# Kernel tuning notes

Hardware: AMD Instinct MI355X
Metric: run time of the kernel (lower is better)

Reference implementation:

```python
import jax, jax.numpy as jnp
import numpy as np

NUM_HEADS = 16
ROPE_BASE = 10000.0


def _rope_tables(seq_len, head_dim, dtype=jnp.float32):
    # Standard RoPE: inv_freq over even dims, cos/sin of shape [seq, head_dim]
    inv_freq = 1.0 / (ROPE_BASE ** (jnp.arange(0, head_dim, 2, dtype=jnp.float32) / head_dim))
    freqs = jnp.arange(seq_len, dtype=jnp.float32)[:, None] * inv_freq[None, :]  # [S, hd/2]
    emb = jnp.concatenate([freqs, freqs], axis=-1)  # [S, hd]
    return jnp.cos(emb).astype(dtype), jnp.sin(emb).astype(dtype)


def _apply_rope(t, cos, sin):
    # t: [B, H, S, hd]; cos/sin: [S, hd]
    half = t.shape[-1] // 2
    rot = jnp.concatenate([-t[..., half:], t[..., :half]], axis=-1)
    return t * cos[None, None, :, :] + rot * sin[None, None, :, :]


def setup_inputs() -> dict:
    key = jax.random.key(0)
    ks = jax.random.split(key, 7)
    B, S, D, L = 2, 2048, 2048, 256
    sc = lambda fan_in: 1.0 / np.sqrt(fan_in)
    return {
        "x": jax.random.normal(ks[0], (B, S, D), jnp.float32),
        "wq": jax.random.normal(ks[1], (D, D), jnp.float32) * sc(D),
        "wdkv": jax.random.normal(ks[2], (L, D), jnp.float32) * sc(D),
        "wuk": jax.random.normal(ks[3], (D, L), jnp.float32) * sc(L),
        "wuv": jax.random.normal(ks[4], (D, L), jnp.float32) * sc(L),
        "wo": jax.random.normal(ks[5], (D, D), jnp.float32) * sc(D),
        "bo": jnp.zeros((D,), jnp.float32),
    }


def reference(x, wq, wdkv, wuk, wuv, wo, bo):
    B, S, D = x.shape
    H = NUM_HEADS
    hd = wq.shape[0] // H

    # Projections (torch nn.Linear: y = x @ W.T)
    q = jnp.einsum("bsd,ed->bse", x, wq)          # [B, S, D]
    latent = jnp.einsum("bsd,ld->bsl", x, wdkv)   # [B, S, L]
    k = jnp.einsum("bsl,el->bse", latent, wuk)    # [B, S, D]
    v = jnp.einsum("bsl,el->bse", latent, wuv)    # [B, S, D]

    split = lambda t: t.reshape(B, S, H, hd).transpose(0, 2, 1, 3)  # [B, H, S, hd]
    q, k, v = split(q), split(k), split(v)

    cos, sin = _rope_tables(S, hd, x.dtype)
    q = _apply_rope(q, cos, sin)
    k = _apply_rope(k, cos, sin)

    scores = jnp.einsum("bhqd,bhkd->bhqk", q, k) / jnp.sqrt(jnp.asarray(hd, x.dtype))
    causal = jnp.tril(jnp.ones((S, S), bool))
    scores = jnp.where(causal[None, None], scores, jnp.asarray(-jnp.inf, x.dtype))
    attn = jax.nn.softmax(scores, axis=-1)

    ctx = jnp.einsum("bhqk,bhkd->bhqd", attn, v)
    ctx = ctx.transpose(0, 2, 1, 3).reshape(B, S, H * hd)
    return jnp.einsum("bse,oe->bso", ctx, wo) + bo
```

## Files before the change

### kernel.cpp

```cpp
#include <hip/hip_runtime.h>
#include <hip/hip_bf16.h>

typedef __bf16 bf16;
typedef __bf16 bf16x8 __attribute__((ext_vector_type(8)));
typedef __bf16 bf16x4 __attribute__((ext_vector_type(4)));
typedef float  f32x4  __attribute__((ext_vector_type(4)));
typedef float  f32x16 __attribute__((ext_vector_type(16)));
typedef unsigned int u32x4 __attribute__((ext_vector_type(4)));

#define D_MODEL 2048
#define SEQ     2048
#define BATCH   2
#define NHEAD   16
#define HDIM    128
#define LATENT  256
#define BROWS   SEQ

typedef __attribute__((address_space(1))) void gvoid;
typedef __attribute__((address_space(3))) void svoid;

__device__ __forceinline__ void gld16(const bf16* g, bf16* l) {
  __builtin_amdgcn_global_load_lds((gvoid*)(void*)g, (svoid*)l, 16, 0, 0);
}

__device__ __forceinline__ f32x4 mfma16(bf16x8 a, bf16x8 b, f32x4 c) {
  return __builtin_amdgcn_mfma_f32_16x16x32_bf16(a, b, c, 0, 0, 0);
}
__device__ __forceinline__ f32x16 mfma32(bf16x8 a, bf16x8 b, f32x16 c) {
  return __builtin_amdgcn_mfma_f32_32x32x16_bf16(a, b, c, 0, 0, 0);
}

__device__ __forceinline__ unsigned cvt_pk_bf16(float lo, float hi) {
  unsigned r;
  asm("v_cvt_pk_bf16_f32 %0, %1, %2" : "=v"(r) : "v"(lo), "v"(hi));
  return r;
}

__device__ __forceinline__ float fw(float v) {
  union { float f; unsigned u; } x; x.f = v;
  if ((x.u & 0x7f800000u) == 0x7f800000u) return 0.f;
  return v;
}

template<typename T>
__device__ __forceinline__ bf16x8 ld_cvt8(const T* p);
template<>
__device__ __forceinline__ bf16x8 ld_cvt8<float>(const float* p) {
  const float4 a = *(const float4*)p;
  const float4 b = *(const float4*)(p + 4);
  bf16x8 r;
  r[0] = (bf16)a.x; r[1] = (bf16)a.y; r[2] = (bf16)a.z; r[3] = (bf16)a.w;
  r[4] = (bf16)b.x; r[5] = (bf16)b.y; r[6] = (bf16)b.z; r[7] = (bf16)b.w;
  return r;
}
template<>
__device__ __forceinline__ bf16x8 ld_cvt8<bf16>(const bf16* p) {
  return *(const bf16x8*)p;
}

template<typename TC>
__device__ __forceinline__ void st_c(TC* p, float v);
template<> __device__ __forceinline__ void st_c<bf16>(bf16* p, float v)   { *p = (bf16)v; }
template<> __device__ __forceinline__ void st_c<float>(float* p, float v) { *p = v; }

__global__ __launch_bounds__(256)
void cvt_bf16(const float* __restrict__ in, bf16* __restrict__ out, int n8)
{
  int i = blockIdx.x * 256 + threadIdx.x;
  if (i >= n8) return;
  const float4 a = ((const float4*)in)[2 * i];
  const float4 b = ((const float4*)in)[2 * i + 1];
  bf16x8 r;
  r[0] = (bf16)a.x; r[1] = (bf16)a.y; r[2] = (bf16)a.z; r[3] = (bf16)a.w;
  r[4] = (bf16)b.x; r[5] = (bf16)b.y; r[6] = (bf16)b.z; r[7] = (bf16)b.w;
  ((bf16x8*)out)[i] = r;
}

template<typename TA, typename TW, typename TC, int BIAS, int TRANSC>
__global__ __launch_bounds__(256)
void gemm_nt(const TA* __restrict__ A, const TW* __restrict__ W,
             TC* __restrict__ C, const float* __restrict__ bias,
             int M, int N, int K)
{
  const int t    = threadIdx.x;
  const int wave = t >> 6, lane = t & 63;
  const int quad = lane >> 4, l16 = lane & 15;
  const int wr = (wave >> 1) * 64, wc = (wave & 1) * 64;
  const int am0 = blockIdx.x * 128;
  const int bn0 = blockIdx.y * 128;

  __shared__ __align__(16) bf16 As[128][40];
  __shared__ __align__(16) bf16 Bs[128][40];

  const f32x4 fzero = {0.f, 0.f, 0.f, 0.f};
  f32x4 acc[4][4];
#pragma unroll
  for (int i = 0; i < 4; i++)
#pragma unroll
    for (int j = 0; j < 4; j++) acc[i][j] = fzero;

  const int srow = t >> 2;
  const int scol = (t & 3) * 8;

  for (int k0 = 0; k0 < K; k0 += 32) {
#pragma unroll
    for (int c = 0; c < 2; c++) {
      int row = srow + c * 64;
      *(bf16x8*)(&As[row][scol]) =
        ld_cvt8<TA>(A + (size_t)(am0 + row) * K + k0 + scol);
      *(bf16x8*)(&Bs[row][scol]) =
        ld_cvt8<TW>(W + (size_t)(bn0 + row) * K + k0 + scol);
    }
    __syncthreads();

    bf16x8 af[4], bfr[4];
#pragma unroll
    for (int i = 0; i < 4; i++)
      af[i]  = *(const bf16x8*)(&As[wr + i*16 + l16][quad*8]);
#pragma unroll
    for (int j = 0; j < 4; j++)
      bfr[j] = *(const bf16x8*)(&Bs[wc + j*16 + l16][quad*8]);
#pragma unroll
    for (int i = 0; i < 4; i++)
#pragma unroll
      for (int j = 0; j < 4; j++)
        acc[i][j] = mfma16(af[i], bfr[j], acc[i][j]);
    __syncthreads();
  }

#pragma unroll
  for (int i = 0; i < 4; i++) {
#pragma unroll
    for (int j = 0; j < 4; j++) {
      int col = bn0 + wc + j*16 + l16;
      float bv = 0.f;
      if (BIAS) bv = bias[col];
#pragma unroll
      for (int r = 0; r < 4; r++) {
        int row = am0 + wr + i*16 + quad*4 + r;
        if (TRANSC)
          st_c<TC>(&C[(size_t)col * M + row], fw(acc[i][j][r] + bv));
        else
          st_c<TC>(&C[(size_t)row * N + col], fw(acc[i][j][r] + bv));
      }
    }
  }
}

template<typename TC, int BIAS, int TRANSC>
__global__ __launch_bounds__(256)
void gemm_bb(const bf16* __restrict__ A, const bf16* __restrict__ W,
             TC* __restrict__ C, const float* __restrict__ bias,
             int M, int N, int K)
{
  const int t    = threadIdx.x;
  const int wave = t >> 6, lane = t & 63;
  const int quad = lane >> 4, l16 = lane & 15;
  const int wr = (wave >> 1) * 64, wc = (wave & 1) * 64;
  const int am0 = blockIdx.x * 128;
  const int bn0 = blockIdx.y * 128;

  __shared__ __align__(16) bf16 As[128 * 32];
  __shared__ __align__(16) bf16 Bs[128 * 32];

  const f32x4 fzero = {0.f, 0.f, 0.f, 0.f};
  f32x4 acc[4][4];
#pragma unroll
  for (int i = 0; i < 4; i++)
#pragma unroll
    for (int j = 0; j < 4; j++) acc[i][j] = fzero;

  for (int k0 = 0; k0 < K; k0 += 32) {
#pragma unroll
    for (int c = 0; c < 2; c++) {
      int e   = c * 256 + t;
      int row = e >> 2, col = (e & 3) * 8;
      gld16(A + (size_t)(am0 + row) * K + k0 + col, As + e * 8);
      gld16(W + (size_t)(bn0 + row) * K + k0 + col, Bs + e * 8);
    }
    __syncthreads();

    bf16x8 af[4], bfr[4];
#pragma unroll
    for (int i = 0; i < 4; i++)
      af[i]  = *(const bf16x8*)(As + (size_t)(wr + i*16 + l16) * 32 + quad * 8);
#pragma unroll
    for (int j = 0; j < 4; j++)
      bfr[j] = *(const bf16x8*)(Bs + (size_t)(wc + j*16 + l16) * 32 + quad * 8);
#pragma unroll
    for (int i = 0; i < 4; i++)
#pragma unroll
      for (int j = 0; j < 4; j++)
        acc[i][j] = mfma16(af[i], bfr[j], acc[i][j]);
    __syncthreads();
  }

#pragma unroll
  for (int i = 0; i < 4; i++) {
#pragma unroll
    for (int j = 0; j < 4; j++) {
      int col = bn0 + wc + j*16 + l16;
      float bv = 0.f;
      if (BIAS) bv = bias[col];
#pragma unroll
      for (int r = 0; r < 4; r++) {
        int row = am0 + wr + i*16 + quad*4 + r;
        if (TRANSC)
          st_c<TC>(&C[(size_t)col * M + row], fw(acc[i][j][r] + bv));
        else
          st_c<TC>(&C[(size_t)row * N + col], fw(acc[i][j][r] + bv));
      }
    }
  }
}

template<typename TC, int BIAS, int TRANSC>
__global__ __launch_bounds__(256)
void gemm_bf(const bf16* __restrict__ A, const float* __restrict__ W,
             TC* __restrict__ C, const float* __restrict__ bias,
             int M, int N, int K)
{
  const int t    = threadIdx.x;
  const int wave = t >> 6, lane = t & 63;
  const int quad = lane >> 4, l16 = lane & 15;
  const int wr = (wave >> 1) * 64, wc = (wave & 1) * 64;
  const int am0 = blockIdx.x * 128;
  const int bn0 = blockIdx.y * 128;

  __shared__ __align__(16) bf16 As[128 * 32];
  __shared__ __align__(16) bf16 Bs[128][40];

  const f32x4 fzero = {0.f, 0.f, 0.f, 0.f};
  f32x4 acc[4][4];
#pragma unroll
  for (int i = 0; i < 4; i++)
#pragma unroll
    for (int j = 0; j < 4; j++) acc[i][j] = fzero;

  const int srow = t >> 2;
  const int scol = (t & 3) * 8;

  for (int k0 = 0; k0 < K; k0 += 32) {
#pragma unroll
    for (int c = 0; c < 2; c++) {
      int e   = c * 256 + t;
      int row = e >> 2, col = (e & 3) * 8;
      gld16(A + (size_t)(am0 + row) * K + k0 + col, As + e * 8);
      int brow = srow + c * 64;
      *(bf16x8*)(&Bs[brow][scol]) =
        ld_cvt8<float>(W + (size_t)(bn0 + brow) * K + k0 + scol);
    }
    __syncthreads();

    bf16x8 af[4], bfr[4];
#pragma unroll
    for (int i = 0; i < 4; i++)
      af[i]  = *(const bf16x8*)(As + (size_t)(wr + i*16 + l16) * 32 + quad * 8);
#pragma unroll
    for (int j = 0; j < 4; j++)
      bfr[j] = *(const bf16x8*)(&Bs[wc + j*16 + l16][quad*8]);
#pragma unroll
    for (int i = 0; i < 4; i++)
#pragma unroll
      for (int j = 0; j < 4; j++)
        acc[i][j] = mfma16(af[i], bfr[j], acc[i][j]);
    __syncthreads();
  }

#pragma unroll
  for (int i = 0; i < 4; i++) {
#pragma unroll
    for (int j = 0; j < 4; j++) {
      int col = bn0 + wc + j*16 + l16;
      float bv = 0.f;
      if (BIAS) bv = bias[col];
#pragma unroll
      for (int r = 0; r < 4; r++) {
        int row = am0 + wr + i*16 + quad*4 + r;
        if (TRANSC)
          st_c<TC>(&C[(size_t)col * M + row], fw(acc[i][j][r] + bv));
        else
          st_c<TC>(&C[(size_t)row * N + col], fw(acc[i][j][r] + bv));
      }
    }
  }
}

template<int SPLITK>
__global__ __launch_bounds__(256)
void gemm_bf_sk(const bf16* __restrict__ A, const float* __restrict__ W,
                float* __restrict__ Cp, int M, int N, int K)
{
  const int t    = threadIdx.x;
  const int wave = t >> 6, lane = t & 63;
  const int quad = lane >> 4, l16 = lane & 15;
  const int wr = (wave >> 1) * 64, wc = (wave & 1) * 64;
  const int am0 = blockIdx.x * 128;
  const int bn0 = blockIdx.y * 128;
  const int kbeg = blockIdx.z * (K / SPLITK);
  const int kend = kbeg + K / SPLITK;

  __shared__ __align__(16) bf16 As[128 * 32];
  __shared__ __align__(16) bf16 Bs[128][40];

  const f32x4 fzero = {0.f, 0.f, 0.f, 0.f};
  f32x4 acc[4][4];
#pragma unroll
  for (int i = 0; i < 4; i++)
#pragma unroll
    for (int j = 0; j < 4; j++) acc[i][j] = fzero;

  const int srow = t >> 2;
  const int scol = (t & 3) * 8;

  for (int k0 = kbeg; k0 < kend; k0 += 32) {
#pragma unroll
    for (int c = 0; c < 2; c++) {
      int e   = c * 256 + t;
      int row = e >> 2, col = (e & 3) * 8;
      gld16(A + (size_t)(am0 + row) * K + k0 + col, As + e * 8);
      int brow = srow + c * 64;
      *(bf16x8*)(&Bs[brow][scol]) =
        ld_cvt8<float>(W + (size_t)(bn0 + brow) * K + k0 + scol);
    }
    __syncthreads();

    bf16x8 af[4], bfr[4];
#pragma unroll
    for (int i = 0; i < 4; i++)
      af[i]  = *(const bf16x8*)(As + (size_t)(wr + i*16 + l16) * 32 + quad * 8);
#pragma unroll
    for (int j = 0; j < 4; j++)
      bfr[j] = *(const bf16x8*)(&Bs[wc + j*16 + l16][quad*8]);
#pragma unroll
    for (int i = 0; i < 4; i++)
#pragma unroll
      for (int j = 0; j < 4; j++)
        acc[i][j] = mfma16(af[i], bfr[j], acc[i][j]);
    __syncthreads();
  }

  float* Cb = Cp + (size_t)blockIdx.z * M * N;
#pragma unroll
  for (int i = 0; i < 4; i++)
#pragma unroll
    for (int j = 0; j < 4; j++) {
      int col = bn0 + wc + j*16 + l16;
#pragma unroll
      for (int r = 0; r < 4; r++) {
        int row = am0 + wr + i*16 + quad*4 + r;
        Cb[(size_t)row * N + col] = acc[i][j][r];
      }
    }
}

template<int SPLITK>
__global__ __launch_bounds__(256)
void reduce_sk(const float* __restrict__ Cp, bf16* __restrict__ out, int MN)
{
  int i4 = (blockIdx.x * 256 + threadIdx.x) * 4;
  if (i4 >= MN) return;
  float4 s = *(const float4*)(Cp + i4);
#pragma unroll
  for (int k = 1; k < SPLITK; k++) {
    float4 p = *(const float4*)(Cp + (size_t)k * MN + i4);
    s.x += p.x; s.y += p.y; s.z += p.z; s.w += p.w;
  }
  bf16x4 o;
  o[0] = (bf16)fw(s.x); o[1] = (bf16)fw(s.y);
  o[2] = (bf16)fw(s.z); o[3] = (bf16)fw(s.w);
  *(bf16x4*)(out + i4) = o;
}

__global__ __launch_bounds__(256)
void rope_kernel(bf16* __restrict__ Q, bf16* __restrict__ Kr)
{
  int idx = blockIdx.x * 256 + threadIdx.x;
  int j   = idx & 63;
  int h   = (idx >> 6) & 15;
  int row = idx >> 10;
  int s   = row & (SEQ - 1);

  float invf = exp2f(-0.2076205059304601f * (float)j);
  float ang  = (float)s * invf;
  float c = cosf(ang), si = sinf(ang);

  size_t base = (size_t)row * D_MODEL + h * HDIM;
  float q1 = (float)Q[base + j], q2 = (float)Q[base + j + 64];
  Q[base + j]      = (bf16)(q1 * c - q2 * si);
  Q[base + j + 64] = (bf16)(q2 * c + q1 * si);
  float k1 = (float)Kr[base + j], k2 = (float)Kr[base + j + 64];
  Kr[base + j]      = (bf16)(k1 * c - k2 * si);
  Kr[base + j + 64] = (bf16)(k2 * c + k1 * si);
}

__global__ __launch_bounds__(256, 2)
void flash_attn(const bf16* __restrict__ Q, const bf16* __restrict__ Kc,
                const bf16* __restrict__ VT, bf16* __restrict__ O, int ldVT)
{
  const int L    = blockIdx.x;
  const int half = L >> 8;
  const int Mn   = L & 255;
  const int h    = Mn >> 4;
  const int a    = Mn & 15;
  const int qt   = half ? 15 - a : a;
  const int b    = half;
  const int t    = threadIdx.x;
  const int wave = t >> 6, lane = t & 63;
  const int m31  = lane & 31, hi = lane >> 5;
  const int rowbase = b * SEQ;

  __shared__ __align__(16) bf16 Ks[64 * 128];
  __shared__ __align__(16) bf16 Vs[128 * 64];

  bf16x8 qf[8];
  {
    const bf16* qp = Q + (size_t)(rowbase + qt*128 + wave*32 + m31) * D_MODEL
                   + h * HDIM + hi * 8;
#pragma unroll
    for (int dk = 0; dk < 8; dk++)
      qf[dk] = *(const bf16x8*)(qp + dk * 16);
  }

  f32x16 oacc[4];
#pragma unroll
  for (int db = 0; db < 4; db++)
#pragma unroll
    for (int i = 0; i < 16; i++) oacc[db][i] = 0.f;
  float lsum = 0.f;

  const float SC2 = 0.12752051581562927f;

  const int ktmax = 2*qt + 1;
  const bf16* kbase0 = Kc + (size_t)rowbase * D_MODEL + h * HDIM;
  const bf16* vbase0 = VT + (size_t)(h*HDIM) * ldVT + rowbase;

  bf16x8 kr[4], vr[4];
#pragma unroll
  for (int c = 0; c < 4; c++) {
    int e = c*256 + t;
    kr[c] = *(const bf16x8*)(kbase0 + (size_t)(e >> 4) * D_MODEL + (e & 15) * 8);
    vr[c] = *(const bf16x8*)(vbase0 + (size_t)(e >> 3) * ldVT + (e & 7) * 8);
  }

  for (int kt = 0; kt <= ktmax; kt++) {
#pragma unroll
    for (int c = 0; c < 4; c++) {
      int e = c*256 + t;
      int krow = e >> 4, kch = e & 15;
      *(bf16x8*)(Ks + krow * 128 + ((kch ^ (krow & 7)) * 8)) = kr[c];
      int vrow = e >> 3, vch = e & 7;
      *(bf16x8*)(Vs + vrow * 64  + ((vch ^ (vrow & 7)) * 8)) = vr[c];
    }
    __syncthreads();

    if (kt < ktmax) {
      const bf16* kb = kbase0 + (size_t)((kt+1)*64) * D_MODEL;
      const bf16* vb = vbase0 + (kt+1)*64;
#pragma unroll
      for (int c = 0; c < 4; c++) {
        int e = c*256 + t;
        kr[c] = *(const bf16x8*)(kb + (size_t)(e >> 4) * D_MODEL + (e & 15) * 8);
        vr[c] = *(const bf16x8*)(vb + (size_t)(e >> 3) * ldVT + (e & 7) * 8);
      }
    }

    const int kvoff = kt*64 - qt*128;
    const bool activ = (kvoff < 0) | (kvoff <= wave*32 + 31);

    if (activ) {
      unsigned pb[4][4];
#pragma unroll
      for (int kb = 0; kb < 2; kb++) {
        f32x16 s;
#pragma unroll
        for (int i = 0; i < 16; i++) s[i] = 0.f;
        const int krow = kb*32 + m31;
        const bf16* ksrow = Ks + krow * 128;
        const int swz = (krow & 7);
#pragma unroll
        for (int dk = 0; dk < 8; dk++) {
          bf16x8 kf = *(const bf16x8*)(ksrow + (((dk*2 + hi) ^ swz) * 8));
          s = mfma32(kf, qf[dk], s);
        }

        float p[16];
        const int kq = kvoff + kb*32 + 4*hi - (wave*32 + m31);
#pragma unroll
        for (int r = 0; r < 16; r++) {
          float v = s[r] * SC2;
          const int kk = (r & 3) + 8 * (r >> 2);
          if (kvoff >= 0 && (kq + kk) > 0) v = -1e30f;
          float e2 = exp2f(v);
          lsum += e2;
          p[r] = e2;
        }

#pragma unroll
        for (int c = 0; c < 2; c++) {
          unsigned a0 = cvt_pk_bf16(p[(2*c)*4 + 0],   p[(2*c)*4 + 1]);
          unsigned a1 = cvt_pk_bf16(p[(2*c)*4 + 2],   p[(2*c)*4 + 3]);
          unsigned b0 = cvt_pk_bf16(p[(2*c+1)*4 + 0], p[(2*c+1)*4 + 1]);
          unsigned b1 = cvt_pk_bf16(p[(2*c+1)*4 + 2], p[(2*c+1)*4 + 3]);
          asm("v_permlane32_swap_b32 %0, %1" : "+v"(a0), "+v"(b0));
          asm("v_permlane32_swap_b32 %0, %1" : "+v"(a1), "+v"(b1));
          pb[kb*2 + c][0] = a0; pb[kb*2 + c][1] = a1;
          pb[kb*2 + c][2] = b0; pb[kb*2 + c][3] = b1;
        }
      }

#pragma unroll
      for (int db = 0; db < 4; db++) {
        const int vrow = db*32 + m31;
        const bf16* vsrow = Vs + vrow * 64;
        const int swz = (vrow & 7);
#pragma unroll
        for (int kc = 0; kc < 4; kc++) {
          bf16x8 vf = *(const bf16x8*)(vsrow + (((kc*2 + hi) ^ swz) * 8));
          u32x4 w = {pb[kc][0], pb[kc][1], pb[kc][2], pb[kc][3]};
          oacc[db] = mfma32(vf, __builtin_bit_cast(bf16x8, w), oacc[db]);
        }
      }
    }
    __syncthreads();
  }

  const float ltot = lsum + __shfl_xor(lsum, 32, 64);
  const float invl = 1.f / ltot;
  const size_t ob = (size_t)(rowbase + qt*128 + wave*32 + m31) * D_MODEL + h * HDIM;
#pragma unroll
  for (int db = 0; db < 4; db++) {
#pragma unroll
    for (int q2 = 0; q2 < 4; q2++) {
      bf16x4 o4;
#pragma unroll
      for (int rr = 0; rr < 4; rr++)
        o4[rr] = (bf16)(oacc[db][q2*4 + rr] * invl);
      *(bf16x4*)(O + ob + db*32 + q2*8 + hi*4) = o4;
    }
  }
}

extern "C" void kernel_launch(void* const* d_in, const int* in_sizes, int n_in,
                              void* d_out, int out_size, void* d_ws, size_t ws_size,
                              hipStream_t stream)
{
  const float* x    = (const float*)d_in[0];
  const float* wq   = (const float*)d_in[1];
  const float* wdkv = (const float*)d_in[2];
  const float* wuk  = (const float*)d_in[3];
  const float* wuv  = (const float*)d_in[4];
  const float* wo   = (const float*)d_in[5];
  const float* bo   = (const float*)d_in[6];
  float* out = (float*)d_out;

  const size_t MTOT = (size_t)BATCH * BROWS;
  const size_t NEED_FULL = (MTOT * D_MODEL + (size_t)D_MODEL * MTOT
                          + MTOT * LATENT) * sizeof(bf16);

  if (ws_size >= NEED_FULL) {
    bf16* Kb  = (bf16*)d_ws;
    bf16* VTb = Kb  + MTOT * D_MODEL;
    bf16* Lt  = VTb + (size_t)D_MODEL * MTOT;
    bf16* wqb = Kb;
    bf16* wob = VTb;
    float* Pp = (float*)d_ws;
    bf16* sb  = (bf16*)out;
    bf16* xb  = sb + MTOT * D_MODEL;

    cvt_bf16<<<(int)(MTOT * D_MODEL / 8 / 256), 256, 0, stream>>>(x,  xb,  (int)(MTOT * D_MODEL / 8));
    cvt_bf16<<<(int)((size_t)D_MODEL * D_MODEL / 8 / 256), 256, 0, stream>>>(wq, wqb, (int)((size_t)D_MODEL * D_MODEL / 8));

    gemm_bb<bf16, 0, 0><<<dim3(32, 16), 256, 0, stream>>>(xb, wqb, sb, nullptr, (int)MTOT, D_MODEL, D_MODEL);

    gemm_bf_sk<8><<<dim3(32, 2, 8), 256, 0, stream>>>(xb, wdkv, Pp, (int)MTOT, LATENT, D_MODEL);
    reduce_sk<8><<<(int)(MTOT * LATENT / 4 / 256), 256, 0, stream>>>(Pp, Lt, (int)(MTOT * LATENT));
    gemm_bf<bf16, 0, 0><<<dim3(32, 16), 256, 0, stream>>>(Lt, wuk,  Kb,  nullptr, (int)MTOT, D_MODEL, LATENT);
    gemm_bf<bf16, 0, 1><<<dim3(32, 16), 256, 0, stream>>>(Lt, wuv,  VTb, nullptr, (int)MTOT, D_MODEL, LATENT);

    rope_kernel<<<(int)(MTOT * NHEAD * 64) / 256, 256, 0, stream>>>(sb, Kb);

    flash_attn<<<dim3(512), 256, 0, stream>>>(sb, Kb, VTb, sb, (int)MTOT);

    cvt_bf16<<<(int)((size_t)D_MODEL * D_MODEL / 8 / 256), 256, 0, stream>>>(wo, wob, (int)((size_t)D_MODEL * D_MODEL / 8));
    hipMemcpyAsync(Kb, sb, MTOT * D_MODEL * sizeof(bf16),
                   hipMemcpyDeviceToDevice, stream);

    gemm_bb<float, 1, 0><<<dim3(32, 16), 256, 0, stream>>>(Kb, wob, out, bo, (int)MTOT, D_MODEL, D_MODEL);
  } else {
    bf16* Kb  = (bf16*)d_ws;
    bf16* VTb = Kb + (size_t)BROWS * D_MODEL;

    for (int b = 0; b < BATCH; b++) {
      const float* xb   = x   + (size_t)b * BROWS * D_MODEL;
      float*       outb = out + (size_t)b * BROWS * D_MODEL;
      bf16*        sb   = (bf16*)outb;

      gemm_nt<float, float, bf16, 0, 0><<<dim3(16, 2),  256, 0, stream>>>(xb, wdkv, sb,  nullptr, BROWS, LATENT,  D_MODEL);
      gemm_nt<bf16,  float, bf16, 0, 0><<<dim3(16, 16), 256, 0, stream>>>(sb, wuk,  Kb,  nullptr, BROWS, D_MODEL, LATENT);
      gemm_nt<bf16,  float, bf16, 0, 1><<<dim3(16, 16), 256, 0, stream>>>(sb, wuv,  VTb, nullptr, BROWS, D_MODEL, LATENT);
      gemm_nt<float, float, bf16, 0, 0><<<dim3(16, 16), 256, 0, stream>>>(xb, wq,   sb,  nullptr, BROWS, D_MODEL, D_MODEL);

      rope_kernel<<<(BROWS * NHEAD * 64) / 256, 256, 0, stream>>>(sb, Kb);

      flash_attn<<<dim3(256), 256, 0, stream>>>(sb, Kb, VTb, sb, BROWS);

      hipMemcpyAsync(Kb, sb, (size_t)BROWS * D_MODEL * sizeof(bf16),
                     hipMemcpyDeviceToDevice, stream);
      gemm_nt<bf16, float, float, 1, 0><<<dim3(16, 16), 256, 0, stream>>>(Kb, wo, outb, bo, BROWS, D_MODEL, D_MODEL);
    }
  }
}
```

Measured before the change: 373.5 us.

## Pair complementary causal query tiles in one 512-thread flash-attention block

Each flash-attention block now has 8 waves covering two query tiles, qt=a and qt=15-a, of the same head and batch. They share one K/V tile stream loaded into LDS up to the larger tile's range, which halves total K/V global loads and balances causal work within a block. MFMA sections are wrapped in s_setprio to favour matrix issue, and the row-sum accumulation is split into four partial sums to shorten the dependency chain. The cost is that waves of the shorter tile sit idle through the later iterations while still hitting barriers, and each block uses more registers.

```diff
diff --git a/kernel.cpp b/kernel.cpp
--- a/kernel.cpp
+++ b/kernel.cpp
@@ -394,19 +394,20 @@
   Kr[base + j + 64] = (bf16)(k2 * c + k1 * si);
 }
 
-__global__ __launch_bounds__(256, 2)
+__global__ __launch_bounds__(512, 2)
 void flash_attn(const bf16* __restrict__ Q, const bf16* __restrict__ Kc,
                 const bf16* __restrict__ VT, bf16* __restrict__ O, int ldVT)
 {
   const int L    = blockIdx.x;
-  const int half = L >> 8;
-  const int Mn   = L & 255;
-  const int h    = Mn >> 4;
-  const int a    = Mn & 15;
-  const int qt   = half ? 15 - a : a;
-  const int b    = half;
+  const int b    = L >> 7;
+  const int r7   = L & 127;
+  const int h    = r7 & 15;
+  const int a    = r7 >> 4;
   const int t    = threadIdx.x;
   const int wave = t >> 6, lane = t & 63;
+  const int g    = wave >> 2;
+  const int wsub = wave & 3;
+  const int qt   = g ? 15 - a : a;
   const int m31  = lane & 31, hi = lane >> 5;
   const int rowbase = b * SEQ;
 
@@ -415,7 +416,7 @@
 
   bf16x8 qf[8];
   {
-    const bf16* qp = Q + (size_t)(rowbase + qt*128 + wave*32 + m31) * D_MODEL
+    const bf16* qp = Q + (size_t)(rowbase + qt*128 + wsub*32 + m31) * D_MODEL
                    + h * HDIM + hi * 8;
 #pragma unroll
     for (int dk = 0; dk < 8; dk++)
@@ -427,26 +428,26 @@
   for (int db = 0; db < 4; db++)
 #pragma unroll
     for (int i = 0; i < 16; i++) oacc[db][i] = 0.f;
-  float lsum = 0.f;
+  float ls[4] = {0.f, 0.f, 0.f, 0.f};
 
   const float SC2 = 0.12752051581562927f;
 
-  const int ktmax = 2*qt + 1;
+  const int ktmax = 31 - 2*a;
   const bf16* kbase0 = Kc + (size_t)rowbase * D_MODEL + h * HDIM;
   const bf16* vbase0 = VT + (size_t)(h*HDIM) * ldVT + rowbase;
 
-  bf16x8 kr[4], vr[4];
-#pragma unroll
-  for (int c = 0; c < 4; c++) {
-    int e = c*256 + t;
+  bf16x8 kr[2], vr[2];
+#pragma unroll
+  for (int c = 0; c < 2; c++) {
+    int e = c*512 + t;
     kr[c] = *(const bf16x8*)(kbase0 + (size_t)(e >> 4) * D_MODEL + (e & 15) * 8);
     vr[c] = *(const bf16x8*)(vbase0 + (size_t)(e >> 3) * ldVT + (e & 7) * 8);
   }
 
   for (int kt = 0; kt <= ktmax; kt++) {
 #pragma unroll
-    for (int c = 0; c < 4; c++) {
-      int e = c*256 + t;
+    for (int c = 0; c < 2; c++) {
+      int e = c*512 + t;
       int krow = e >> 4, kch = e & 15;
       *(bf16x8*)(Ks + krow * 128 + ((kch ^ (krow & 7)) * 8)) = kr[c];
       int vrow = e >> 3, vch = e & 7;
@@ -458,15 +459,15 @@
       const bf16* kb = kbase0 + (size_t)((kt+1)*64) * D_MODEL;
       const bf16* vb = vbase0 + (kt+1)*64;
 #pragma unroll
-      for (int c = 0; c < 4; c++) {
-        int e = c*256 + t;
+      for (int c = 0; c < 2; c++) {
+        int e = c*512 + t;
         kr[c] = *(const bf16x8*)(kb + (size_t)(e >> 4) * D_MODEL + (e & 15) * 8);
         vr[c] = *(const bf16x8*)(vb + (size_t)(e >> 3) * ldVT + (e & 7) * 8);
       }
     }
 
     const int kvoff = kt*64 - qt*128;
-    const bool activ = (kvoff < 0) | (kvoff <= wave*32 + 31);
+    const bool activ = (kvoff < 0) | (kvoff <= wsub*32 + 31);
 
     if (activ) {
       unsigned pb[4][4];
@@ -478,21 +479,23 @@
         const int krow = kb*32 + m31;
         const bf16* ksrow = Ks + krow * 128;
         const int swz = (krow & 7);
+        __builtin_amdgcn_s_setprio(1);
 #pragma unroll
         for (int dk = 0; dk < 8; dk++) {
           bf16x8 kf = *(const bf16x8*)(ksrow + (((dk*2 + hi) ^ swz) * 8));
           s = mfma32(kf, qf[dk], s);
         }
+        __builtin_amdgcn_s_setprio(0);
 
         float p[16];
-        const int kq = kvoff + kb*32 + 4*hi - (wave*32 + m31);
+        const int kq = kvoff + kb*32 + 4*hi - (wsub*32 + m31);
 #pragma unroll
         for (int r = 0; r < 16; r++) {
           float v = s[r] * SC2;
           const int kk = (r & 3) + 8 * (r >> 2);
           if (kvoff >= 0 && (kq + kk) > 0) v = -1e30f;
           float e2 = exp2f(v);
-          lsum += e2;
+          ls[r & 3] += e2;
           p[r] = e2;
         }
 
@@ -509,6 +512,7 @@
         }
       }
 
+      __builtin_amdgcn_s_setprio(1);
 #pragma unroll
       for (int db = 0; db < 4; db++) {
         const int vrow = db*32 + m31;
@@ -521,13 +525,15 @@
           oacc[db] = mfma32(vf, __builtin_bit_cast(bf16x8, w), oacc[db]);
         }
       }
-    }
-    __syncthreads();
-  }
-
+      __builtin_amdgcn_s_setprio(0);
+    }
+    __syncthreads();
+  }
+
+  const float lsum = (ls[0] + ls[1]) + (ls[2] + ls[3]);
   const float ltot = lsum + __shfl_xor(lsum, 32, 64);
   const float invl = 1.f / ltot;
-  const size_t ob = (size_t)(rowbase + qt*128 + wave*32 + m31) * D_MODEL + h * HDIM;
+  const size_t ob = (size_t)(rowbase + qt*128 + wsub*32 + m31) * D_MODEL + h * HDIM;
 #pragma unroll
   for (int db = 0; db < 4; db++) {
 #pragma unroll
@@ -580,7 +586,7 @@
 
     rope_kernel<<<(int)(MTOT * NHEAD * 64) / 256, 256, 0, stream>>>(sb, Kb);
 
-    flash_attn<<<dim3(512), 256, 0, stream>>>(sb, Kb, VTb, sb, (int)MTOT);
+    flash_attn<<<dim3(256), 512, 0, stream>>>(sb, Kb, VTb, sb, (int)MTOT);
 
     cvt_bf16<<<(int)((size_t)D_MODEL * D_MODEL / 8 / 256), 256, 0, stream>>>(wo, wob, (int)((size_t)D_MODEL * D_MODEL / 8));
     hipMemcpyAsync(Kb, sb, MTOT * D_MODEL * sizeof(bf16),
@@ -603,7 +609,7 @@
 
       rope_kernel<<<(BROWS * NHEAD * 64) / 256, 256, 0, stream>>>(sb, Kb);
 
-      flash_attn<<<dim3(256), 256, 0, stream>>>(sb, Kb, VTb, sb, BROWS);
+      flash_attn<<<dim3(128), 512, 0, stream>>>(sb, Kb, VTb, sb, BROWS);
 
       hipMemcpyAsync(Kb, sb, (size_t)BROWS * D_MODEL * sizeof(bf16),
                      hipMemcpyDeviceToDevice, stream);
```

New measurement: 382.0 us. +2.3%, slower.

## Double-buffer K/V tiles in flash attention with one barrier per iteration

Applied to the files above, without the earlier changes.

Gives the K and V shared-memory tiles two buffers, so the next tile is written to the alternate buffer after compute and only one __syncthreads is needed per iteration instead of two. Loads two tiles ahead in registers. Also raises wave priority around the MFMA blocks, splits the softmax row-sum into four partial accumulators to shorten the dependency chain, and reorders block-to-(head, q-tile) mapping so that neighbouring blocks share a q-tile across heads. The cost is double the LDS use (64KB per block), which may limit the two-blocks-per-CU occupancy target.

```diff
diff --git a/kernel.cpp b/kernel.cpp
--- a/kernel.cpp
+++ b/kernel.cpp
@@ -401,8 +401,8 @@
   const int L    = blockIdx.x;
   const int half = L >> 8;
   const int Mn   = L & 255;
-  const int h    = Mn >> 4;
-  const int a    = Mn & 15;
+  const int h    = Mn & 15;
+  const int a    = Mn >> 4;
   const int qt   = half ? 15 - a : a;
   const int b    = half;
   const int t    = threadIdx.x;
@@ -410,8 +410,8 @@
   const int m31  = lane & 31, hi = lane >> 5;
   const int rowbase = b * SEQ;
 
-  __shared__ __align__(16) bf16 Ks[64 * 128];
-  __shared__ __align__(16) bf16 Vs[128 * 64];
+  __shared__ __align__(16) bf16 Ks[2][64 * 128];
+  __shared__ __align__(16) bf16 Vs[2][128 * 64];
 
   bf16x8 qf[8];
   {
@@ -427,7 +427,7 @@
   for (int db = 0; db < 4; db++)
 #pragma unroll
     for (int i = 0; i < 16; i++) oacc[db][i] = 0.f;
-  float lsum = 0.f;
+  float ls[4] = {0.f, 0.f, 0.f, 0.f};
 
   const float SC2 = 0.12752051581562927f;
 
@@ -442,28 +442,30 @@
     kr[c] = *(const bf16x8*)(kbase0 + (size_t)(e >> 4) * D_MODEL + (e & 15) * 8);
     vr[c] = *(const bf16x8*)(vbase0 + (size_t)(e >> 3) * ldVT + (e & 7) * 8);
   }
-
-  for (int kt = 0; kt <= ktmax; kt++) {
+#pragma unroll
+  for (int c = 0; c < 4; c++) {
+    int e = c*256 + t;
+    int krow = e >> 4, kch = e & 15;
+    *(bf16x8*)(&Ks[0][krow * 128 + ((kch ^ (krow & 7)) * 8)]) = kr[c];
+    int vrow = e >> 3, vch = e & 7;
+    *(bf16x8*)(&Vs[0][vrow * 64  + ((vch ^ (vrow & 7)) * 8)]) = vr[c];
+  }
+  __syncthreads();
+  if (ktmax >= 1) {
+    const bf16* kb = kbase0 + (size_t)64 * D_MODEL;
+    const bf16* vb = vbase0 + 64;
 #pragma unroll
     for (int c = 0; c < 4; c++) {
       int e = c*256 + t;
-      int krow = e >> 4, kch = e & 15;
-      *(bf16x8*)(Ks + krow * 128 + ((kch ^ (krow & 7)) * 8)) = kr[c];
-      int vrow = e >> 3, vch = e & 7;
-      *(bf16x8*)(Vs + vrow * 64  + ((vch ^ (vrow & 7)) * 8)) = vr[c];
-    }
-    __syncthreads();
-
-    if (kt < ktmax) {
-      const bf16* kb = kbase0 + (size_t)((kt+1)*64) * D_MODEL;
-      const bf16* vb = vbase0 + (kt+1)*64;
-#pragma unroll
-      for (int c = 0; c < 4; c++) {
-        int e = c*256 + t;
-        kr[c] = *(const bf16x8*)(kb + (size_t)(e >> 4) * D_MODEL + (e & 15) * 8);
-        vr[c] = *(const bf16x8*)(vb + (size_t)(e >> 3) * ldVT + (e & 7) * 8);
-      }
-    }
+      kr[c] = *(const bf16x8*)(kb + (size_t)(e >> 4) * D_MODEL + (e & 15) * 8);
+      vr[c] = *(const bf16x8*)(vb + (size_t)(e >> 3) * ldVT + (e & 7) * 8);
+    }
+  }
+
+  for (int kt = 0; kt <= ktmax; kt++) {
+    const int cur = kt & 1;
+    const bf16* Kcur = &Ks[cur][0];
+    const bf16* Vcur = &Vs[cur][0];
 
     const int kvoff = kt*64 - qt*128;
     const bool activ = (kvoff < 0) | (kvoff <= wave*32 + 31);
@@ -476,13 +478,15 @@
 #pragma unroll
         for (int i = 0; i < 16; i++) s[i] = 0.f;
         const int krow = kb*32 + m31;
-        const bf16* ksrow = Ks + krow * 128;
+        const bf16* ksrow = Kcur + krow * 128;
         const int swz = (krow & 7);
+        __builtin_amdgcn_s_setprio(1);
 #pragma unroll
         for (int dk = 0; dk < 8; dk++) {
           bf16x8 kf = *(const bf16x8*)(ksrow + (((dk*2 + hi) ^ swz) * 8));
           s = mfma32(kf, qf[dk], s);
         }
+        __builtin_amdgcn_s_setprio(0);
 
         float p[16];
         const int kq = kvoff + kb*32 + 4*hi - (wave*32 + m31);
@@ -492,7 +496,7 @@
           const int kk = (r & 3) + 8 * (r >> 2);
           if (kvoff >= 0 && (kq + kk) > 0) v = -1e30f;
           float e2 = exp2f(v);
-          lsum += e2;
+          ls[r & 3] += e2;
           p[r] = e2;
         }
 
@@ -509,10 +513,11 @@
         }
       }
 
+      __builtin_amdgcn_s_setprio(1);
 #pragma unroll
       for (int db = 0; db < 4; db++) {
         const int vrow = db*32 + m31;
-        const bf16* vsrow = Vs + vrow * 64;
+        const bf16* vsrow = Vcur + vrow * 64;
         const int swz = (vrow & 7);
 #pragma unroll
         for (int kc = 0; kc < 4; kc++) {
@@ -521,10 +526,35 @@
           oacc[db] = mfma32(vf, __builtin_bit_cast(bf16x8, w), oacc[db]);
         }
       }
-    }
-    __syncthreads();
-  }
-
+      __builtin_amdgcn_s_setprio(0);
+    }
+
+    if (kt < ktmax) {
+      bf16* Kn = &Ks[cur ^ 1][0];
+      bf16* Vn = &Vs[cur ^ 1][0];
+#pragma unroll
+      for (int c = 0; c < 4; c++) {
+        int e = c*256 + t;
+        int krow = e >> 4, kch = e & 15;
+        *(bf16x8*)(Kn + krow * 128 + ((kch ^ (krow & 7)) * 8)) = kr[c];
+        int vrow = e >> 3, vch = e & 7;
+        *(bf16x8*)(Vn + vrow * 64  + ((vch ^ (vrow & 7)) * 8)) = vr[c];
+      }
+      if (kt + 1 < ktmax) {
+        const bf16* kb = kbase0 + (size_t)((kt+2)*64) * D_MODEL;
+        const bf16* vb = vbase0 + (kt+2)*64;
+#pragma unroll
+        for (int c = 0; c < 4; c++) {
+          int e = c*256 + t;
+          kr[c] = *(const bf16x8*)(kb + (size_t)(e >> 4) * D_MODEL + (e & 15) * 8);
+          vr[c] = *(const bf16x8*)(vb + (size_t)(e >> 3) * ldVT + (e & 7) * 8);
+        }
+      }
+    }
+    __syncthreads();
+  }
+
+  const float lsum = (ls[0] + ls[1]) + (ls[2] + ls[3]);
   const float ltot = lsum + __shfl_xor(lsum, 32, 64);
   const float invl = 1.f / ltot;
   const size_t ob = (size_t)(rowbase + qt*128 + wave*32 + m31) * D_MODEL + h * HDIM;
```

Measured after the change: 376.7 us. No clear change (+0.8%).
